# Performance work log

Hardware: AMD Instinct MI355X
Metric: run time of the kernel (lower is better)

The kernel has to match this reference:

```python
import jax, jax.numpy as jnp
import numpy as np

N_SRC = 100000
N_DST = 100000
E = 1600000
IN_DIM = 128
OUT_DIM = 64
NEG_SLOPE = 0.01  # torch F.leaky_relu default


def setup_inputs() -> dict:
    key = jax.random.key(0)
    ks = jax.random.split(key, 7)
    g = np.sqrt(2.0)  # relu gain used in xavier init; scale only, not exactness-critical
    return {
        "h_src": jax.random.normal(ks[0], (N_SRC, IN_DIM), jnp.float32),
        "h_dst": jax.random.normal(ks[1], (N_DST, IN_DIM), jnp.float32),
        "src_idx": jax.random.randint(ks[2], (E,), 0, N_SRC, jnp.int32),
        "dst_idx": jax.random.randint(ks[3], (E,), 0, N_DST, jnp.int32),
        "W_src": (jax.random.normal(ks[4], (OUT_DIM, IN_DIM), jnp.float32) * (g / np.sqrt(IN_DIM))),
        "W_dst": (jax.random.normal(ks[5], (OUT_DIM, IN_DIM), jnp.float32) * (g / np.sqrt(IN_DIM))),
        "attn_w": (jax.random.normal(ks[6], (1, 2 * OUT_DIM), jnp.float32) * (g / np.sqrt(2 * OUT_DIM))),
        "item_user": 0,
    }


def reference(h_src, h_dst, src_idx, dst_idx, W_src, W_dst, attn_w, item_user):
    # node projections (fc_src / fc_dst, no bias)
    z_src = h_src @ W_src.T                      # [N_src, OUT]
    if item_user:
        z_src = jax.nn.softplus(z_src)
    z_dst = h_dst @ W_dst.T                      # [N_dst, OUT]

    # attn_fc(cat(z_src_e, z_dst_e)) == z_src @ a_l + z_dst @ a_r (precompute per node)
    a_l = attn_w[0, :OUT_DIM]
    a_r = attn_w[0, OUT_DIM:]
    el = z_src @ a_l                             # [N_src]
    er = z_dst @ a_r                             # [N_dst]

    e = jax.nn.leaky_relu(el[src_idx] + er[dst_idx], NEG_SLOPE)  # [E]

    # segment softmax over edges grouped by dst (stable: subtract per-dst max)
    m = jax.ops.segment_max(e, dst_idx, num_segments=N_DST)      # [N_dst], -inf for empty
    ex = jnp.exp(e - m[dst_idx])                                  # [E]
    denom = jax.ops.segment_sum(ex, dst_idx, num_segments=N_DST)  # [N_dst]
    alpha = ex / denom[dst_idx]                                   # [E]

    # weighted scatter-sum of source messages; empty dst nodes get zeros (DGL default)
    msgs = alpha[:, None] * z_src[src_idx]                        # [E, OUT]
    h_out = jax.ops.segment_sum(msgs, dst_idx, num_segments=N_DST)  # [N_dst, OUT]
    return h_out
```

## Files before the change

### kernel.cpp

```cpp
#include <hip/hip_runtime.h>
#include <math.h>

#define NSRC 100000
#define NDST 100000
#define NE   1600000
#define IND  128
#define OUTD 64
#define SLOPE 0.01f
#define CAP  48

#define FILL_BLOCKS 782
#define ER_BLOCKS   782
#define ZTILES      1563
#define P1_BLOCKS (FILL_BLOCKS + ER_BLOCKS + ZTILES)

typedef _Float16       f16x8 __attribute__((ext_vector_type(8)));
typedef float          f32x4 __attribute__((ext_vector_type(4)));
typedef unsigned short u16x8 __attribute__((ext_vector_type(8)));

__device__ __forceinline__ float softplus_f(float x) {
    return (x > 20.f) ? x : log1pf(__expf(x));
}
__device__ __forceinline__ unsigned short f2bf(float f) {
    unsigned u = __float_as_uint(f);
    return (unsigned short)((u + 0x7FFFu + ((u >> 16) & 1u)) >> 16);
}
__device__ __forceinline__ float bf2f(unsigned short h) {
    return __uint_as_float(((unsigned)h) << 16);
}

__device__ __forceinline__ void zsrc_body(float* vsrc, int tile,
                                          const float* __restrict__ h_src,
                                          const float* __restrict__ W_src,
                                          const float* __restrict__ attn_w,
                                          int iu,
                                          unsigned short* __restrict__ z16,
                                          float* __restrict__ el) {
    const int t = threadIdx.x;
    if (t < IND) {
        float a = 0.f;
#pragma unroll 8
        for (int o = 0; o < OUTD; ++o)
            a = fmaf(W_src[o * IND + t], attn_w[o], a);
        vsrc[t] = a;
    }
    __syncthreads();

    const int w = t >> 6, l = t & 63;
    const int r = l & 15, q = l >> 4;
    const int rowA  = tile * 64 + w * 16 + r;
    const int rowAc = (rowA < NSRC) ? rowA : (NSRC - 1);

    f32x4 acc[4];
#pragma unroll
    for (int c = 0; c < 4; ++c) acc[c] = (f32x4)0.f;
    float elp = 0.f;

#pragma unroll
    for (int ks = 0; ks < 4; ++ks) {
        const float* ap = h_src + rowAc * IND + ks * 32 + q * 8;
        float4 a0 = *(const float4*)ap;
        float4 a1 = *(const float4*)(ap + 4);
        const float* vp = vsrc + ks * 32 + q * 8;
        float4 v0 = *(const float4*)vp;
        float4 v1 = *(const float4*)(vp + 4);
        elp = fmaf(a0.x, v0.x, elp); elp = fmaf(a0.y, v0.y, elp);
        elp = fmaf(a0.z, v0.z, elp); elp = fmaf(a0.w, v0.w, elp);
        elp = fmaf(a1.x, v1.x, elp); elp = fmaf(a1.y, v1.y, elp);
        elp = fmaf(a1.z, v1.z, elp); elp = fmaf(a1.w, v1.w, elp);
        f16x8 af;
        af[0] = (_Float16)a0.x; af[1] = (_Float16)a0.y;
        af[2] = (_Float16)a0.z; af[3] = (_Float16)a0.w;
        af[4] = (_Float16)a1.x; af[5] = (_Float16)a1.y;
        af[6] = (_Float16)a1.z; af[7] = (_Float16)a1.w;
#pragma unroll
        for (int c = 0; c < 4; ++c) {
            const float* bp = W_src + (16 * c + r) * IND + ks * 32 + q * 8;
            float4 b0 = *(const float4*)bp;
            float4 b1 = *(const float4*)(bp + 4);
            f16x8 bf;
            bf[0] = (_Float16)b0.x; bf[1] = (_Float16)b0.y;
            bf[2] = (_Float16)b0.z; bf[3] = (_Float16)b0.w;
            bf[4] = (_Float16)b1.x; bf[5] = (_Float16)b1.y;
            bf[6] = (_Float16)b1.z; bf[7] = (_Float16)b1.w;
            acc[c] = __builtin_amdgcn_mfma_f32_16x16x32_f16(af, bf, acc[c], 0, 0, 0);
        }
    }

    if (!iu) {
        elp += __shfl_xor(elp, 16);
        elp += __shfl_xor(elp, 32);
        if (q == 0 && rowA < NSRC) el[rowA] = elp;
    } else {
#pragma unroll
        for (int c = 0; c < 4; ++c)
#pragma unroll
            for (int j = 0; j < 4; ++j) acc[c][j] = softplus_f(acc[c][j]);
        float ac0 = attn_w[r], ac1 = attn_w[16 + r], ac2 = attn_w[32 + r], ac3 = attn_w[48 + r];
#pragma unroll
        for (int j = 0; j < 4; ++j) {
            float s = fmaf(acc[0][j], ac0, fmaf(acc[1][j], ac1,
                      fmaf(acc[2][j], ac2, acc[3][j] * ac3)));
            s += __shfl_xor(s, 1); s += __shfl_xor(s, 2);
            s += __shfl_xor(s, 4); s += __shfl_xor(s, 8);
            const int row = tile * 64 + w * 16 + q * 4 + j;
            if (r == 0 && row < NSRC) el[row] = s;
        }
    }

    const int rowD0 = tile * 64 + w * 16 + q * 4;
#pragma unroll
    for (int j = 0; j < 4; ++j) {
        const int row = rowD0 + j;
        if (row < NSRC) {
#pragma unroll
            for (int c = 0; c < 4; ++c)
                z16[row * OUTD + 16 * c + r] = f2bf(acc[c][j]);
        }
    }
}

__device__ __forceinline__ void er_body(float* v, int eb,
                                        const float* __restrict__ h_dst,
                                        const float* __restrict__ W_dst,
                                        const float* __restrict__ attn_w,
                                        float* __restrict__ er) {
    const int t = threadIdx.x;
    if (t < IND) {
        float a = 0.f;
#pragma unroll 8
        for (int o = 0; o < OUTD; ++o)
            a = fmaf(W_dst[o * IND + t], attn_w[OUTD + o], a);
        v[t] = a;
    }
    __syncthreads();
    const int wv = t >> 6, l = t & 63, hh = l >> 5, c = l & 31;
    float4 vv = *(const float4*)(v + c * 4);
    const int row0 = eb * 128;
#pragma unroll 4
    for (int p = 0; p < 16; ++p) {
        int row = row0 + p * 8 + wv * 2 + hh;
        if (row < NDST) {
            float4 x = *(const float4*)(h_dst + row * IND + c * 4);
            float s = fmaf(x.x, vv.x, fmaf(x.y, vv.y, fmaf(x.z, vv.z, x.w * vv.w)));
            s += __shfl_xor(s, 16); s += __shfl_xor(s, 8);
            s += __shfl_xor(s, 4);  s += __shfl_xor(s, 2);
            s += __shfl_xor(s, 1);
            if (c == 0) er[row] = s;
        }
    }
}

__device__ __forceinline__ void fill_body(int fb, const int* __restrict__ src,
                                          const int* __restrict__ dst,
                                          int* __restrict__ cnt,
                                          int* __restrict__ slot) {
    int j = fb * 2048 + threadIdx.x;
#pragma unroll 2
    for (int it = 0; it < 8; ++it, j += 256) {
        if (j < NE) {
            int d = dst[j];
            int s = src[j];
            int p = atomicAdd(&cnt[d], 1);
            if (p < CAP) slot[d * CAP + p] = s;
        }
    }
}

__global__ __launch_bounds__(256) void k_p1(
        const float* __restrict__ h_src, const float* __restrict__ W_src,
        const float* __restrict__ attn_w, const int* __restrict__ item_user,
        const float* __restrict__ h_dst, const float* __restrict__ W_dst,
        const int* __restrict__ src_idx, const int* __restrict__ dst_idx,
        unsigned short* __restrict__ z16, float* __restrict__ el,
        float* __restrict__ er, int* __restrict__ cnt,
        int* __restrict__ slot) {
    __shared__ float smem[IND];
    const int b = blockIdx.x;
    if (b < FILL_BLOCKS) {
        fill_body(b, src_idx, dst_idx, cnt, slot);
    } else if (b < FILL_BLOCKS + ER_BLOCKS) {
        er_body(smem, b - FILL_BLOCKS, h_dst, W_dst, attn_w, er);
    } else {
        zsrc_body(smem, b - FILL_BLOCKS - ER_BLOCKS, h_src, W_src, attn_w,
                  *item_user, z16, el);
    }
}

__global__ __launch_bounds__(256) void k_aggregate(
        const int* __restrict__ cnt, const int* __restrict__ slot,
        const float* __restrict__ el, const float* __restrict__ er,
        const unsigned short* __restrict__ z16, float* __restrict__ out) {
    const int wave = threadIdx.x >> 6, lane = threadIdx.x & 63;
    const int g = lane >> 3, gl = lane & 7;
    const int d = blockIdx.x * 4 + wave;
    int deg = cnt[d];
    deg = (deg < 0) ? 0 : ((deg > CAP) ? CAP : deg);
    const float er_d = er[d];

    float acc[8];
#pragma unroll
    for (int k = 0; k < 8; ++k) acc[k] = 0.f;
    float dsum = 0.f;

    for (int base = 0; base < deg; base += 8) {
        int i = base + g;
        if (i < deg) {
            int s = slot[d * CAP + i];
            s = ((unsigned)s < (unsigned)NSRC) ? s : 0;
            float e = el[s] + er_d;
            e = (e > 0.f) ? e : SLOPE * e;
            float ex = __expf(e);
            u16x8 zz = *(const u16x8*)(z16 + s * OUTD + gl * 8);
#pragma unroll
            for (int k = 0; k < 8; ++k) acc[k] = fmaf(ex, bf2f(zz[k]), acc[k]);
            dsum += ex;
        }
    }
#pragma unroll
    for (int off = 8; off <= 32; off <<= 1) {
        dsum += __shfl_xor(dsum, off);
#pragma unroll
        for (int k = 0; k < 8; ++k) acc[k] += __shfl_xor(acc[k], off);
    }
    if (g == 0) {
        float inv = (deg > 0 && dsum > 0.f) ? 1.f / dsum : 0.f;
        float4 o0 = float4{acc[0] * inv, acc[1] * inv, acc[2] * inv, acc[3] * inv};
        float4 o1 = float4{acc[4] * inv, acc[5] * inv, acc[6] * inv, acc[7] * inv};
        *(float4*)(out + d * OUTD + gl * 8)     = o0;
        *(float4*)(out + d * OUTD + gl * 8 + 4) = o1;
    }
}

extern "C" void kernel_launch(void* const* d_in, const int* in_sizes, int n_in,
                              void* d_out, int out_size, void* d_ws, size_t ws_size,
                              hipStream_t stream) {
    const float* h_src   = (const float*)d_in[0];
    const float* h_dst   = (const float*)d_in[1];
    const int*   src_idx = (const int*)d_in[2];
    const int*   dst_idx = (const int*)d_in[3];
    const float* W_src   = (const float*)d_in[4];
    const float* W_dst   = (const float*)d_in[5];
    const float* attn_w  = (const float*)d_in[6];
    const int*   item_u  = (const int*)d_in[7];
    float* out = (float*)d_out;

    char* ws = (char*)d_ws;
    unsigned short* z16 = (unsigned short*)(ws);
    float* el   = (float*)(ws + 12800000);
    float* er   = (float*)(ws + 13200000);
    int*   cnt  = (int*)  (ws + 13600000);
    int*   slot = (int*)  (ws + 14000000);

    hipMemsetAsync(cnt, 0, 400000, stream);

    k_p1       <<<P1_BLOCKS, 256, 0, stream>>>(h_src, W_src, attn_w, item_u,
                                               h_dst, W_dst, src_idx, dst_idx,
                                               z16, el, er, cnt, slot);
    k_aggregate<<<25000,     256, 0, stream>>>(cnt, slot, el, er, z16, out);
}
```

Baseline: 307.9 us.

## Use nontemporal streaming loads, vectorize edge fill, and precompute edge weights per lane

Streaming reads of h_src, h_dst and the edge index arrays now use nontemporal loads, so data read once is kept from displacing the gathered tables in cache. The fill phase has each thread load 8 consecutive edges with vector loads and issue all atomics before the slot writes, which raises memory-level parallelism. The aggregate kernel loads all slot indices and el values once per wave (one per lane) and computes exp and the denominator sum up front. The gather loop then only broadcasts index and weight through shuffles, removing repeated dependent loads from the critical path, at the cost of extra shuffles and a full-wave reduction.

```diff
diff --git a/kernel.cpp b/kernel.cpp
--- a/kernel.cpp
+++ b/kernel.cpp
@@ -17,6 +17,8 @@
 typedef _Float16       f16x8 __attribute__((ext_vector_type(8)));
 typedef float          f32x4 __attribute__((ext_vector_type(4)));
 typedef unsigned short u16x8 __attribute__((ext_vector_type(8)));
+typedef int            i32x4 __attribute__((ext_vector_type(4)));
+typedef float          f32v4 __attribute__((ext_vector_type(4)));
 
 __device__ __forceinline__ float softplus_f(float x) {
     return (x > 20.f) ? x : log1pf(__expf(x));
@@ -27,6 +29,14 @@
 }
 __device__ __forceinline__ float bf2f(unsigned short h) {
     return __uint_as_float(((unsigned)h) << 16);
+}
+__device__ __forceinline__ float4 ntload4f(const float* p) {
+    f32v4 v = __builtin_nontemporal_load((const f32v4*)p);
+    return float4{v.x, v.y, v.z, v.w};
+}
+__device__ __forceinline__ int4 ntload4i(const int* p) {
+    i32x4 v = __builtin_nontemporal_load((const i32x4*)p);
+    return int4{v.x, v.y, v.z, v.w};
 }
 
 __device__ __forceinline__ void zsrc_body(float* vsrc, int tile,
@@ -59,8 +69,8 @@
 #pragma unroll
     for (int ks = 0; ks < 4; ++ks) {
         const float* ap = h_src + rowAc * IND + ks * 32 + q * 8;
-        float4 a0 = *(const float4*)ap;
-        float4 a1 = *(const float4*)(ap + 4);
+        float4 a0 = ntload4f(ap);
+        float4 a1 = ntload4f(ap + 4);
         const float* vp = vsrc + ks * 32 + q * 8;
         float4 v0 = *(const float4*)vp;
         float4 v1 = *(const float4*)(vp + 4);
@@ -141,7 +151,7 @@
     for (int p = 0; p < 16; ++p) {
         int row = row0 + p * 8 + wv * 2 + hh;
         if (row < NDST) {
-            float4 x = *(const float4*)(h_dst + row * IND + c * 4);
+            float4 x = ntload4f(h_dst + row * IND + c * 4);
             float s = fmaf(x.x, vv.x, fmaf(x.y, vv.y, fmaf(x.z, vv.z, x.w * vv.w)));
             s += __shfl_xor(s, 16); s += __shfl_xor(s, 8);
             s += __shfl_xor(s, 4);  s += __shfl_xor(s, 2);
@@ -155,16 +165,28 @@
                                           const int* __restrict__ dst,
                                           int* __restrict__ cnt,
                                           int* __restrict__ slot) {
-    int j = fb * 2048 + threadIdx.x;
-#pragma unroll 2
-    for (int it = 0; it < 8; ++it, j += 256) {
-        if (j < NE) {
-            int d = dst[j];
-            int s = src[j];
-            int p = atomicAdd(&cnt[d], 1);
-            if (p < CAP) slot[d * CAP + p] = s;
-        }
-    }
+    const int j0 = fb * 2048 + threadIdx.x * 8;
+    if (j0 >= NE) return;
+    int4 d0 = ntload4i(dst + j0);
+    int4 d1 = ntload4i(dst + j0 + 4);
+    int4 s0 = ntload4i(src + j0);
+    int4 s1 = ntload4i(src + j0 + 4);
+    int p0 = atomicAdd(&cnt[d0.x], 1);
+    int p1 = atomicAdd(&cnt[d0.y], 1);
+    int p2 = atomicAdd(&cnt[d0.z], 1);
+    int p3 = atomicAdd(&cnt[d0.w], 1);
+    int p4 = atomicAdd(&cnt[d1.x], 1);
+    int p5 = atomicAdd(&cnt[d1.y], 1);
+    int p6 = atomicAdd(&cnt[d1.z], 1);
+    int p7 = atomicAdd(&cnt[d1.w], 1);
+    if (p0 < CAP) slot[d0.x * CAP + p0] = s0.x;
+    if (p1 < CAP) slot[d0.y * CAP + p1] = s0.y;
+    if (p2 < CAP) slot[d0.z * CAP + p2] = s0.z;
+    if (p3 < CAP) slot[d0.w * CAP + p3] = s0.w;
+    if (p4 < CAP) slot[d1.x * CAP + p4] = s1.x;
+    if (p5 < CAP) slot[d1.y * CAP + p5] = s1.y;
+    if (p6 < CAP) slot[d1.z * CAP + p6] = s1.z;
+    if (p7 < CAP) slot[d1.w * CAP + p7] = s1.w;
 }
 
 __global__ __launch_bounds__(256) void k_p1(
@@ -192,34 +214,41 @@
         const float* __restrict__ el, const float* __restrict__ er,
         const unsigned short* __restrict__ z16, float* __restrict__ out) {
     const int wave = threadIdx.x >> 6, lane = threadIdx.x & 63;
+    const int d = blockIdx.x * 4 + wave;
+    const int degRaw = cnt[d];
+    const float er_d = er[d];
+    int s = 0;
+    if (lane < CAP) s = slot[d * CAP + lane];
+    s = ((unsigned)s < (unsigned)NSRC) ? s : 0;
+    const float elv = el[s];
+
+    const int deg = (degRaw < 0) ? 0 : ((degRaw > CAP) ? CAP : degRaw);
+    float ex = 0.f;
+    if (lane < deg) {
+        float e = elv + er_d;
+        e = (e > 0.f) ? e : SLOPE * e;
+        ex = __expf(e);
+    }
+    float dsum = ex;
+#pragma unroll
+    for (int off = 1; off < 64; off <<= 1) dsum += __shfl_xor(dsum, off);
+
     const int g = lane >> 3, gl = lane & 7;
-    const int d = blockIdx.x * 4 + wave;
-    int deg = cnt[d];
-    deg = (deg < 0) ? 0 : ((deg > CAP) ? CAP : deg);
-    const float er_d = er[d];
-
     float acc[8];
 #pragma unroll
     for (int k = 0; k < 8; ++k) acc[k] = 0.f;
-    float dsum = 0.f;
-
     for (int base = 0; base < deg; base += 8) {
-        int i = base + g;
+        const int i = base + g;
+        const int   si  = __shfl(s, i);
+        const float exi = __shfl(ex, i);
         if (i < deg) {
-            int s = slot[d * CAP + i];
-            s = ((unsigned)s < (unsigned)NSRC) ? s : 0;
-            float e = el[s] + er_d;
-            e = (e > 0.f) ? e : SLOPE * e;
-            float ex = __expf(e);
-            u16x8 zz = *(const u16x8*)(z16 + s * OUTD + gl * 8);
-#pragma unroll
-            for (int k = 0; k < 8; ++k) acc[k] = fmaf(ex, bf2f(zz[k]), acc[k]);
-            dsum += ex;
+            u16x8 zz = *(const u16x8*)(z16 + si * OUTD + gl * 8);
+#pragma unroll
+            for (int k = 0; k < 8; ++k) acc[k] = fmaf(exi, bf2f(zz[k]), acc[k]);
         }
     }
 #pragma unroll
     for (int off = 8; off <= 32; off <<= 1) {
-        dsum += __shfl_xor(dsum, off);
 #pragma unroll
         for (int k = 0; k < 8; ++k) acc[k] += __shfl_xor(acc[k], off);
     }
```

New measurement: 350.3 us. 13.8% more time.

## Pad edge counters to separate cache lines and precompute per-lane edge weights

Applied to the files above, without the earlier changes.

The per-destination counters are padded to a 64-byte stride so that concurrent atomics on different destinations land on separate cache lines. The aggregate kernel now loads all slots and computes the exp weights once per lane in parallel. Each 8-lane group then receives its source index and weight by shuffle instead of recomputing them. The padding makes the memset 16x larger (6.4 MB) and moves the slot buffer to a new workspace offset.

```diff
diff --git a/kernel.cpp b/kernel.cpp
--- a/kernel.cpp
+++ b/kernel.cpp
@@ -8,6 +8,7 @@
 #define OUTD 64
 #define SLOPE 0.01f
 #define CAP  48
+#define CSTR 16
 
 #define FILL_BLOCKS 782
 #define ER_BLOCKS   782
@@ -161,7 +162,7 @@
         if (j < NE) {
             int d = dst[j];
             int s = src[j];
-            int p = atomicAdd(&cnt[d], 1);
+            int p = atomicAdd(&cnt[d * CSTR], 1);
             if (p < CAP) slot[d * CAP + p] = s;
         }
     }
@@ -192,34 +193,40 @@
         const float* __restrict__ el, const float* __restrict__ er,
         const unsigned short* __restrict__ z16, float* __restrict__ out) {
     const int wave = threadIdx.x >> 6, lane = threadIdx.x & 63;
+    const int d = blockIdx.x * 4 + wave;
+    const int degRaw = cnt[d * CSTR];
+    const float er_d = er[d];
+    int s = 0;
+    if (lane < CAP) s = slot[d * CAP + lane];
+    s = ((unsigned)s < (unsigned)NSRC) ? s : 0;
+
+    const int deg = (degRaw < 0) ? 0 : ((degRaw > CAP) ? CAP : degRaw);
+    float ex = 0.f;
+    if (lane < deg) {
+        float e = el[s] + er_d;
+        e = (e > 0.f) ? e : SLOPE * e;
+        ex = __expf(e);
+    }
+    float dsum = ex;
+#pragma unroll
+    for (int off = 1; off < 64; off <<= 1) dsum += __shfl_xor(dsum, off);
+
     const int g = lane >> 3, gl = lane & 7;
-    const int d = blockIdx.x * 4 + wave;
-    int deg = cnt[d];
-    deg = (deg < 0) ? 0 : ((deg > CAP) ? CAP : deg);
-    const float er_d = er[d];
-
     float acc[8];
 #pragma unroll
     for (int k = 0; k < 8; ++k) acc[k] = 0.f;
-    float dsum = 0.f;
-
     for (int base = 0; base < deg; base += 8) {
-        int i = base + g;
+        const int i = base + g;
+        const int   si  = __shfl(s, i);
+        const float exi = __shfl(ex, i);
         if (i < deg) {
-            int s = slot[d * CAP + i];
-            s = ((unsigned)s < (unsigned)NSRC) ? s : 0;
-            float e = el[s] + er_d;
-            e = (e > 0.f) ? e : SLOPE * e;
-            float ex = __expf(e);
-            u16x8 zz = *(const u16x8*)(z16 + s * OUTD + gl * 8);
-#pragma unroll
-            for (int k = 0; k < 8; ++k) acc[k] = fmaf(ex, bf2f(zz[k]), acc[k]);
-            dsum += ex;
+            u16x8 zz = *(const u16x8*)(z16 + si * OUTD + gl * 8);
+#pragma unroll
+            for (int k = 0; k < 8; ++k) acc[k] = fmaf(exi, bf2f(zz[k]), acc[k]);
         }
     }
 #pragma unroll
     for (int off = 8; off <= 32; off <<= 1) {
-        dsum += __shfl_xor(dsum, off);
 #pragma unroll
         for (int k = 0; k < 8; ++k) acc[k] += __shfl_xor(acc[k], off);
     }
@@ -250,9 +257,9 @@
     float* el   = (float*)(ws + 12800000);
     float* er   = (float*)(ws + 13200000);
     int*   cnt  = (int*)  (ws + 13600000);
-    int*   slot = (int*)  (ws + 14000000);
-
-    hipMemsetAsync(cnt, 0, 400000, stream);
+    int*   slot = (int*)  (ws + 20000000);
+
+    hipMemsetAsync(cnt, 0, NDST * CSTR * 4, stream);
 
     k_p1       <<<P1_BLOCKS, 256, 0, stream>>>(h_src, W_src, attn_w, item_u,
                                                h_dst, W_dst, src_idx, dst_idx,
```

New measurement: 305.8 us. Within noise of the previous version (-0.7%).
